# Optimization experiments

Measured on AMD Instinct MI355X. Metric: run time of the kernel, lower is better.

The kernel has to match this reference:

```python
import jax, jax.numpy as jnp
import numpy as np

N_HEAD = 4
GROUPS = 32
EPS = 1e-5


def group_norm(x, scale, bias):
    B, C, H, W = x.shape
    xg = x.reshape(B, GROUPS, C // GROUPS, H, W)
    mu = xg.mean(axis=(2, 3, 4), keepdims=True)
    var = xg.var(axis=(2, 3, 4), keepdims=True)
    xg = (xg - mu) * jax.lax.rsqrt(var + EPS)
    x = xg.reshape(B, C, H, W)
    return x * scale[None, :, None, None] + bias[None, :, None, None]


def setup_inputs() -> dict:
    key = jax.random.key(0)
    k0, k1, k2 = jax.random.split(key, 3)
    B, C, H, W = 2, 64, 64, 64
    x = jax.random.normal(k0, (B, C, H, W), dtype=jnp.float32)
    gn_scale = jnp.ones((C,), dtype=jnp.float32)
    gn_bias = jnp.zeros((C,), dtype=jnp.float32)
    w_qkv = jax.random.normal(k1, (3 * C, C), dtype=jnp.float32) * 0.05  # 1x1 conv, no bias
    w_out = jax.random.normal(k2, (C, C), dtype=jnp.float32) * 0.05     # 1x1 conv
    b_out = jnp.zeros((C,), dtype=jnp.float32)
    return {"x": x, "gn_scale": gn_scale, "gn_bias": gn_bias,
            "w_qkv": w_qkv, "w_out": w_out, "b_out": b_out}


def reference(x, gn_scale, gn_bias, w_qkv, w_out, b_out):
    B, C, H, W = x.shape
    head_dim = C // N_HEAD
    norm = group_norm(x, gn_scale, gn_bias)
    # 1x1 conv == channel matmul
    qkv = jnp.einsum('oc,bchw->bohw', w_qkv, norm)
    qkv = qkv.reshape(B, N_HEAD, head_dim * 3, H, W)
    q, k, v = jnp.split(qkv, 3, axis=2)  # each [B, n, head_dim, H, W]
    # full spatial attention scores, scaled by sqrt(channel) as in source
    attn = jnp.einsum('bnchw,bncyx->bnhwyx', q, k) / jnp.sqrt(jnp.float32(C))
    attn = jax.nn.softmax(attn.reshape(B, N_HEAD, H, W, H * W), axis=-1)
    attn = attn.reshape(B, N_HEAD, H, W, H, W)
    out = jnp.einsum('bnhwyx,bncyx->bnchw', attn, v).reshape(B, C, H, W)
    out = jnp.einsum('oc,bchw->bohw', w_out, out) + b_out[None, :, None, None]
    return out + x
```

## Files before the change

### kernel.cpp

```cpp
#include <hip/hip_runtime.h>
#include <hip/hip_bf16.h>

typedef __attribute__((ext_vector_type(8))) short short8;
typedef __attribute__((ext_vector_type(4))) float f32x4;
typedef __attribute__((ext_vector_type(16))) float f32x16;
typedef __attribute__((ext_vector_type(4))) unsigned int uint4v;

#define DEV static __device__ __forceinline__

DEV unsigned short f2bf(float f){
  unsigned u = __float_as_uint(f);
  u += 0x7fffu + ((u >> 16) & 1u);
  return (unsigned short)(u >> 16);
}

DEV unsigned pack2bf(float a, float b){
  __hip_bfloat162 h = __float22bfloat162_rn(make_float2(a, b));
  unsigned u;
  __builtin_memcpy(&u, &h, 4);
  return u;
}

#define QSCALE 0.180336880111f
#define NSPLIT 8
#define NT 8

__global__ __launch_bounds__(256) void gn_partial_k(const float* __restrict__ x,
                                                    float* __restrict__ gp){
  int blk = blockIdx.x;
  float4 v = ((const float4*)(x + (size_t)blk*1024))[threadIdx.x];
  float s = v.x+v.y+v.z+v.w;
  float q = v.x*v.x+v.y*v.y+v.z*v.z+v.w*v.w;
  #pragma unroll
  for (int off = 1; off < 64; off <<= 1){
    s += __shfl_xor(s, off);
    q += __shfl_xor(q, off);
  }
  __shared__ float red[8];
  int w = threadIdx.x >> 6;
  if ((threadIdx.x & 63) == 0){ red[w*2] = s; red[w*2+1] = q; }
  __syncthreads();
  if (threadIdx.x == 0){
    gp[blk*2+0] = red[0]+red[2]+red[4]+red[6];
    gp[blk*2+1] = red[1]+red[3]+red[5]+red[7];
  }
}

__global__ __launch_bounds__(256) void qkv_k(const float* __restrict__ x,
    const float* __restrict__ gp, const float* __restrict__ gsc,
    const float* __restrict__ gbi, const float* __restrict__ wq,
    unsigned short* __restrict__ q, unsigned short* __restrict__ k,
    unsigned short* __restrict__ vt){
  int b  = blockIdx.x >> 8;
  int s0 = (blockIdx.x & 255) * 16;
  __shared__ float W[192][68];
  __shared__ float A[16][68];
  __shared__ float MS[32][2];
  int t = threadIdx.x;
  for (int i = t; i < 3072; i += 256){
    int o = i >> 4, c4 = (i & 15) * 4;
    *(float4*)&W[o][c4] = ((const float4*)wq)[i];
  }
  if (t < 32){
    float s = 0.f, ss = 0.f;
    #pragma unroll
    for (int i = 0; i < 8; ++i){
      const float* pp = gp + ((b*32 + t)*8 + i)*2;
      s += pp[0]; ss += pp[1];
    }
    float mean = s * (1.f/8192.f);
    MS[t][0] = mean;
    MS[t][1] = rsqrtf(ss * (1.f/8192.f) - mean*mean + 1e-5f);
  }
  __syncthreads();
  {
    int c  = t >> 2;
    int s4 = (t & 3) * 4;
    const float* px = x + ((size_t)b*64 + c)*4096 + s0 + s4;
    float4 v0 = *(const float4*)px;
    float sc = gsc[c] * MS[c>>1][1];
    float bi = gbi[c] - MS[c>>1][0] * sc;
    A[s4+0][c]=v0.x*sc+bi; A[s4+1][c]=v0.y*sc+bi;
    A[s4+2][c]=v0.z*sc+bi; A[s4+3][c]=v0.w*sc+bi;
  }
  __syncthreads();
  int sl = t >> 4, grp = t & 15;
  float acc[12];
  #pragma unroll
  for (int j = 0; j < 12; ++j) acc[j] = 0.f;
  for (int c4 = 0; c4 < 16; ++c4){
    float4 a = *(const float4*)&A[sl][c4*4];
    #pragma unroll
    for (int j = 0; j < 12; ++j){
      float4 wv = *(const float4*)&W[grp + j*16][c4*4];
      acc[j] = fmaf(a.x, wv.x, fmaf(a.y, wv.y, fmaf(a.z, wv.z, fmaf(a.w, wv.w, acc[j]))));
    }
  }
  int s = s0 + sl;
  int slp = (sl & 0x3) | (((sl >> 2) & 1) << 3) | (((sl >> 3) & 1) << 2);
  #pragma unroll
  for (int j = 0; j < 12; ++j){
    int o = grp + j*16;
    int n = o / 48, r = o % 48;
    float val = acc[j];
    if (r < 16){
      q[(((size_t)b*4 + n)*4096 + s)*16 + r] = f2bf(val * QSCALE);
    } else if (r < 32){
      k[(((size_t)b*4 + n)*4096 + s)*16 + r - 16] = f2bf(val);
    } else {
      vt[((size_t)(b*4 + n)*16 + (r - 32))*4096 + s0 + slp] = f2bf(val);
    }
  }
}

__global__ __launch_bounds__(256, 4) void attn_k(const unsigned short* __restrict__ qb,
    const unsigned short* __restrict__ kb, const unsigned short* __restrict__ vt,
    float* __restrict__ part, float* __restrict__ lsums){
  int blk = blockIdx.x;
  int bn = blk & 7;
  int sp = (blk >> 3) & (NSPLIT - 1);
  int qt = blk >> 6;
  int t = threadIdx.x, w = t >> 6, l = t & 63;
  int lq = l & 31, hi = l >> 5;

  const unsigned short* kaddr = kb + ((size_t)bn*4096 + sp*(NT*64) + lq)*16 + hi*8;
  const unsigned short* vaddr = vt + ((size_t)bn*16 + (lq & 15))*4096 + sp*(NT*64) + hi*8;
  bool vld = (lq < 16);
  int qrow = qt*256 + w*64;
  const unsigned short* Qp = qb + ((size_t)bn*4096 + qrow)*16;

  short8 qf0 = *(const short8*)(Qp + (size_t)lq*16 + hi*8);
  short8 qf1 = *(const short8*)(Qp + (size_t)(32 + lq)*16 + hi*8);

  f32x16 O0, O1, zero;
  #pragma unroll
  for (int r = 0; r < 16; ++r){ O0[r] = 0.f; O1[r] = 0.f; zero[r] = 0.f; }

  short8 vsel;
  {
    unsigned short c = (lq == 16) ? (unsigned short)0x3F80 : (unsigned short)0;
    #pragma unroll
    for (int r = 0; r < 8; ++r) vsel[r] = (short)c;
  }

  short8 kf0 = *(const short8*)(kaddr);
  short8 kf1 = *(const short8*)(kaddr + 512);

  #pragma unroll 1
  for (int kt = 0; kt < NT; ++kt){
    short8 v0 = vsel, v1 = vsel, v2 = vsel, v3 = vsel;
    if (vld){
      const unsigned short* va = vaddr + (size_t)kt*64;
      v0 = *(const short8*)(va);
      v1 = *(const short8*)(va + 16);
      v2 = *(const short8*)(va + 32);
      v3 = *(const short8*)(va + 48);
    }
    short8 kn0 = {}, kn1 = {};
    if (kt + 1 < NT){
      const unsigned short* ka = kaddr + (size_t)(kt+1)*1024;
      kn0 = *(const short8*)(ka);
      kn1 = *(const short8*)(ka + 512);
    }

    auto pvstep = [&](f32x16& O, const f32x16& pc, int h8, short8 vf){
      uint4v pw;
      pw[0] = pack2bf(pc[h8+0], pc[h8+1]);
      pw[1] = pack2bf(pc[h8+2], pc[h8+3]);
      pw[2] = pack2bf(pc[h8+4], pc[h8+5]);
      pw[3] = pack2bf(pc[h8+6], pc[h8+7]);
      short8 pa = __builtin_bit_cast(short8, pw);
      O = __builtin_amdgcn_mfma_f32_32x32x16_bf16(pa, vf, O, 0, 0, 0);
    };

    {
      f32x16 sA = __builtin_amdgcn_mfma_f32_32x32x16_bf16(kf0, qf0, zero, 0, 0, 0);
      f32x16 sB = __builtin_amdgcn_mfma_f32_32x32x16_bf16(kf1, qf0, zero, 0, 0, 0);
      #pragma unroll
      for (int r = 0; r < 16; ++r) sA[r] = __builtin_amdgcn_exp2f(sA[r]);
      #pragma unroll
      for (int r = 0; r < 16; ++r) sB[r] = __builtin_amdgcn_exp2f(sB[r]);
      pvstep(O0, sA, 0, v0); pvstep(O0, sA, 8, v1);
      pvstep(O0, sB, 0, v2); pvstep(O0, sB, 8, v3);
    }
    {
      f32x16 sA = __builtin_amdgcn_mfma_f32_32x32x16_bf16(kf0, qf1, zero, 0, 0, 0);
      f32x16 sB = __builtin_amdgcn_mfma_f32_32x32x16_bf16(kf1, qf1, zero, 0, 0, 0);
      #pragma unroll
      for (int r = 0; r < 16; ++r) sA[r] = __builtin_amdgcn_exp2f(sA[r]);
      #pragma unroll
      for (int r = 0; r < 16; ++r) sB[r] = __builtin_amdgcn_exp2f(sB[r]);
      pvstep(O1, sA, 0, v0); pvstep(O1, sA, 8, v1);
      pvstep(O1, sB, 0, v2); pvstep(O1, sB, 8, v3);
    }

    kf0 = kn0; kf1 = kn1;
  }

  float* Op = part + (((size_t)sp*8 + bn)*4096 + qrow)*16;
  size_t lbase = ((size_t)sp*8 + bn)*4096 + qrow;
  #pragma unroll
  for (int r = 0; r < 16; ++r){
    int qr = (r&3) + 8*(r>>2) + 4*hi;
    if (lq < 16){
      __builtin_nontemporal_store(O0[r], &Op[(size_t)qr*16 + lq]);
      __builtin_nontemporal_store(O1[r], &Op[(size_t)(32 + qr)*16 + lq]);
    }
  }
  if (lq == 16){
    #pragma unroll
    for (int r = 0; r < 16; ++r){
      int qr = (r&3) + 8*(r>>2) + 4*hi;
      __builtin_nontemporal_store(O0[r], &lsums[lbase + qr]);
      __builtin_nontemporal_store(O1[r], &lsums[lbase + 32 + qr]);
    }
  }
}

__global__ __launch_bounds__(256) void oproj_k(const float* __restrict__ part,
    const float* __restrict__ lsums, const float* __restrict__ wo,
    const float* __restrict__ bo, const float* __restrict__ x,
    float* __restrict__ out){
  int b  = blockIdx.x >> 8;
  int s0 = (blockIdx.x & 255) * 16;
  __shared__ float W[64][68];
  __shared__ float A[16][68];
  int t = threadIdx.x;
  for (int i = t; i < 1024; i += 256){
    int o = i >> 4, c4 = (i & 15) * 4;
    *(float4*)&W[o][c4] = ((const float4*)wo)[i];
  }
  {
    int sl = t & 15;
    int u  = t >> 4;
    int n = u >> 2, d4 = (u & 3) * 4;
    size_t row = ((size_t)b*4 + n)*4096 + s0 + sl;
    float L = 0.f;
    #pragma unroll
    for (int sp = 0; sp < NSPLIT; ++sp)
      L += __builtin_nontemporal_load(&lsums[(size_t)sp*32768 + row]);
    f32x4 acc = {0.f,0.f,0.f,0.f};
    #pragma unroll
    for (int sp = 0; sp < NSPLIT; ++sp){
      f32x4 u0 = __builtin_nontemporal_load(
          (const f32x4*)(part + ((size_t)sp*32768 + row)*16 + d4));
      acc += u0;
    }
    float inv = 1.f / L;
    A[sl][n*16+d4+0] = acc[0]*inv; A[sl][n*16+d4+1] = acc[1]*inv;
    A[sl][n*16+d4+2] = acc[2]*inv; A[sl][n*16+d4+3] = acc[3]*inv;
  }
  __syncthreads();
  int sl = t & 15, grp = t >> 4;
  float acc[4] = {0.f,0.f,0.f,0.f};
  for (int c4 = 0; c4 < 16; ++c4){
    float4 a = *(const float4*)&A[sl][c4*4];
    #pragma unroll
    for (int j = 0; j < 4; ++j){
      float4 wv = *(const float4*)&W[grp + j*16][c4*4];
      acc[j] = fmaf(a.x, wv.x, fmaf(a.y, wv.y, fmaf(a.z, wv.z, fmaf(a.w, wv.w, acc[j]))));
    }
  }
  int s = s0 + sl;
  #pragma unroll
  for (int j = 0; j < 4; ++j){
    int o = grp + j*16;
    size_t idx = ((size_t)b*64 + o)*4096 + s;
    out[idx] = acc[j] + bo[o] + x[idx];
  }
}

extern "C" void kernel_launch(void* const* d_in, const int* in_sizes, int n_in,
                              void* d_out, int out_size, void* d_ws, size_t ws_size,
                              hipStream_t stream){
  const float* x   = (const float*)d_in[0];
  const float* gsc = (const float*)d_in[1];
  const float* gbi = (const float*)d_in[2];
  const float* wq  = (const float*)d_in[3];
  const float* wo  = (const float*)d_in[4];
  const float* bo  = (const float*)d_in[5];
  float* out = (float*)d_out;

  char* ws = (char*)d_ws;
  float* gp          = (float*)ws;
  unsigned short* q  = (unsigned short*)(ws + 8192);
  unsigned short* k  = (unsigned short*)(ws + 8192 + 1048576);
  unsigned short* vt = (unsigned short*)(ws + 8192 + 2097152);
  float* part        = (float*)(ws + 8192 + 3145728);
  float* lsums       = (float*)(ws + 8192 + 3145728 + 16777216);

  gn_partial_k<<<512,  256, 0, stream>>>(x, gp);
  qkv_k       <<<512,  256, 0, stream>>>(x, gp, gsc, gbi, wq, q, k, vt);
  attn_k      <<<1024, 256, 0, stream>>>(q, k, vt, part, lsums);
  oproj_k     <<<512,  256, 0, stream>>>(part, lsums, wo, bo, x, out);
}
```

Baseline: 58.18 us.

## Stage K/V tiles in LDS and halve the attention key split count

The attention kernel now copies each block's 1024-key K slice and transposed V slice into shared memory, with an XOR swizzle on V. All 8 waves then read K/V from LDS instead of each wave streaming them from global memory. The key split drops from 8 to 4, which halves the partial-output and row-sum buffers that the output projection must reduce. Blocks grow to 512 threads and each wave handles 32 query rows instead of 64. That means one accumulator chain per wave, so there is less MFMA independence to hide latency, and the 64KB of LDS per block limits residency.

```diff
diff --git a/kernel.cpp b/kernel.cpp
--- a/kernel.cpp
+++ b/kernel.cpp
@@ -22,8 +22,8 @@
 }
 
 #define QSCALE 0.180336880111f
-#define NSPLIT 8
-#define NT 8
+#define NSPLIT 4
+#define NT 16
 
 __global__ __launch_bounds__(256) void gn_partial_k(const float* __restrict__ x,
                                                     float* __restrict__ gp){
@@ -113,28 +113,44 @@
   }
 }
 
-__global__ __launch_bounds__(256, 4) void attn_k(const unsigned short* __restrict__ qb,
+__global__ __launch_bounds__(512, 4) void attn_k(const unsigned short* __restrict__ qb,
     const unsigned short* __restrict__ kb, const unsigned short* __restrict__ vt,
     float* __restrict__ part, float* __restrict__ lsums){
   int blk = blockIdx.x;
   int bn = blk & 7;
   int sp = (blk >> 3) & (NSPLIT - 1);
-  int qt = blk >> 6;
+  int qg = blk >> 5;
   int t = threadIdx.x, w = t >> 6, l = t & 63;
   int lq = l & 31, hi = l >> 5;
 
-  const unsigned short* kaddr = kb + ((size_t)bn*4096 + sp*(NT*64) + lq)*16 + hi*8;
-  const unsigned short* vaddr = vt + ((size_t)bn*16 + (lq & 15))*4096 + sp*(NT*64) + hi*8;
-  bool vld = (lq < 16);
-  int qrow = qt*256 + w*64;
-  const unsigned short* Qp = qb + ((size_t)bn*4096 + qrow)*16;
-
-  short8 qf0 = *(const short8*)(Qp + (size_t)lq*16 + hi*8);
-  short8 qf1 = *(const short8*)(Qp + (size_t)(32 + lq)*16 + hi*8);
-
-  f32x16 O0, O1, zero;
-  #pragma unroll
-  for (int r = 0; r < 16; ++r){ O0[r] = 0.f; O1[r] = 0.f; zero[r] = 0.f; }
+  __shared__ unsigned short Klds[16384];
+  __shared__ unsigned short Vlds[16384];
+
+  {
+    const unsigned short* ksrc = kb + ((size_t)bn*4096 + sp*1024)*16;
+    #pragma unroll
+    for (int p = 0; p < 4; ++p){
+      int G = p*512 + t;
+      *(short8*)&Klds[G*8] = *(const short8*)(ksrc + G*8);
+    }
+    const unsigned short* vsrc = vt + (size_t)bn*16*4096 + sp*1024;
+    #pragma unroll
+    for (int p = 0; p < 4; ++p){
+      int G = p*512 + t;
+      int d = G >> 7, gi = G & 127;
+      short8 vv = *(const short8*)(vsrc + (size_t)d*4096 + gi*8);
+      *(short8*)&Vlds[d*1024 + ((gi ^ (d & 7)) * 8)] = vv;
+    }
+  }
+
+  int qrow = qg*256 + w*32;
+  short8 qf = *(const short8*)(qb + ((size_t)bn*4096 + qrow)*16 + (size_t)lq*16 + hi*8);
+
+  __syncthreads();
+
+  f32x16 O, zero;
+  #pragma unroll
+  for (int r = 0; r < 16; ++r){ O[r] = 0.f; zero[r] = 0.f; }
 
   short8 vsel;
   {
@@ -143,27 +159,38 @@
     for (int r = 0; r < 8; ++r) vsel[r] = (short)c;
   }
 
-  short8 kf0 = *(const short8*)(kaddr);
-  short8 kf1 = *(const short8*)(kaddr + 512);
+  int vdrow = (lq & 15);
+  int vxor  = 8 * (vdrow & 7);
+  bool vld = (lq < 16);
+
+  short8 kf0 = *(const short8*)&Klds[(0*64 + 0*32 + lq)*16 + hi*8];
+  short8 kf1 = *(const short8*)&Klds[(0*64 + 1*32 + lq)*16 + hi*8];
 
   #pragma unroll 1
   for (int kt = 0; kt < NT; ++kt){
     short8 v0 = vsel, v1 = vsel, v2 = vsel, v3 = vsel;
     if (vld){
-      const unsigned short* va = vaddr + (size_t)kt*64;
-      v0 = *(const short8*)(va);
-      v1 = *(const short8*)(va + 16);
-      v2 = *(const short8*)(va + 32);
-      v3 = *(const short8*)(va + 48);
+      int base = vdrow*1024 + kt*64 + hi*8;
+      v0 = *(const short8*)&Vlds[(base +  0) ^ vxor];
+      v1 = *(const short8*)&Vlds[(base + 16) ^ vxor];
+      v2 = *(const short8*)&Vlds[(base + 32) ^ vxor];
+      v3 = *(const short8*)&Vlds[(base + 48) ^ vxor];
     }
     short8 kn0 = {}, kn1 = {};
     if (kt + 1 < NT){
-      const unsigned short* ka = kaddr + (size_t)(kt+1)*1024;
-      kn0 = *(const short8*)(ka);
-      kn1 = *(const short8*)(ka + 512);
-    }
-
-    auto pvstep = [&](f32x16& O, const f32x16& pc, int h8, short8 vf){
+      kn0 = *(const short8*)&Klds[((kt+1)*64 + lq)*16 + hi*8];
+      kn1 = *(const short8*)&Klds[((kt+1)*64 + 32 + lq)*16 + hi*8];
+    }
+
+    f32x16 sA = __builtin_amdgcn_mfma_f32_32x32x16_bf16(kf0, qf, zero, 0, 0, 0);
+    f32x16 sB = __builtin_amdgcn_mfma_f32_32x32x16_bf16(kf1, qf, zero, 0, 0, 0);
+
+    #pragma unroll
+    for (int r = 0; r < 16; ++r) sA[r] = __builtin_amdgcn_exp2f(sA[r]);
+    #pragma unroll
+    for (int r = 0; r < 16; ++r) sB[r] = __builtin_amdgcn_exp2f(sB[r]);
+
+    auto pvstep = [&](const f32x16& pc, int h8, short8 vf){
       uint4v pw;
       pw[0] = pack2bf(pc[h8+0], pc[h8+1]);
       pw[1] = pack2bf(pc[h8+2], pc[h8+3]);
@@ -172,27 +199,10 @@
       short8 pa = __builtin_bit_cast(short8, pw);
       O = __builtin_amdgcn_mfma_f32_32x32x16_bf16(pa, vf, O, 0, 0, 0);
     };
-
-    {
-      f32x16 sA = __builtin_amdgcn_mfma_f32_32x32x16_bf16(kf0, qf0, zero, 0, 0, 0);
-      f32x16 sB = __builtin_amdgcn_mfma_f32_32x32x16_bf16(kf1, qf0, zero, 0, 0, 0);
-      #pragma unroll
-      for (int r = 0; r < 16; ++r) sA[r] = __builtin_amdgcn_exp2f(sA[r]);
-      #pragma unroll
-      for (int r = 0; r < 16; ++r) sB[r] = __builtin_amdgcn_exp2f(sB[r]);
-      pvstep(O0, sA, 0, v0); pvstep(O0, sA, 8, v1);
-      pvstep(O0, sB, 0, v2); pvstep(O0, sB, 8, v3);
-    }
-    {
-      f32x16 sA = __builtin_amdgcn_mfma_f32_32x32x16_bf16(kf0, qf1, zero, 0, 0, 0);
-      f32x16 sB = __builtin_amdgcn_mfma_f32_32x32x16_bf16(kf1, qf1, zero, 0, 0, 0);
-      #pragma unroll
-      for (int r = 0; r < 16; ++r) sA[r] = __builtin_amdgcn_exp2f(sA[r]);
-      #pragma unroll
-      for (int r = 0; r < 16; ++r) sB[r] = __builtin_amdgcn_exp2f(sB[r]);
-      pvstep(O1, sA, 0, v0); pvstep(O1, sA, 8, v1);
-      pvstep(O1, sB, 0, v2); pvstep(O1, sB, 8, v3);
-    }
+    pvstep(sA, 0, v0);
+    pvstep(sA, 8, v1);
+    pvstep(sB, 0, v2);
+    pvstep(sB, 8, v3);
 
     kf0 = kn0; kf1 = kn1;
   }
@@ -202,17 +212,13 @@
   #pragma unroll
   for (int r = 0; r < 16; ++r){
     int qr = (r&3) + 8*(r>>2) + 4*hi;
-    if (lq < 16){
-      __builtin_nontemporal_store(O0[r], &Op[(size_t)qr*16 + lq]);
-      __builtin_nontemporal_store(O1[r], &Op[(size_t)(32 + qr)*16 + lq]);
-    }
+    if (lq < 16) __builtin_nontemporal_store(O[r], &Op[(size_t)qr*16 + lq]);
   }
   if (lq == 16){
     #pragma unroll
     for (int r = 0; r < 16; ++r){
       int qr = (r&3) + 8*(r>>2) + 4*hi;
-      __builtin_nontemporal_store(O0[r], &lsums[lbase + qr]);
-      __builtin_nontemporal_store(O1[r], &lsums[lbase + 32 + qr]);
+      __builtin_nontemporal_store(O[r], &lsums[lbase + qr]);
     }
   }
 }
@@ -287,10 +293,10 @@
   unsigned short* k  = (unsigned short*)(ws + 8192 + 1048576);
   unsigned short* vt = (unsigned short*)(ws + 8192 + 2097152);
   float* part        = (float*)(ws + 8192 + 3145728);
-  float* lsums       = (float*)(ws + 8192 + 3145728 + 16777216);
-
-  gn_partial_k<<<512,  256, 0, stream>>>(x, gp);
-  qkv_k       <<<512,  256, 0, stream>>>(x, gp, gsc, gbi, wq, q, k, vt);
-  attn_k      <<<1024, 256, 0, stream>>>(q, k, vt, part, lsums);
-  oproj_k     <<<512,  256, 0, stream>>>(part, lsums, wo, bo, x, out);
-}
+  float* lsums       = (float*)(ws + 8192 + 3145728 + 8388608);
+
+  gn_partial_k<<<512, 256, 0, stream>>>(x, gp);
+  qkv_k       <<<512, 256, 0, stream>>>(x, gp, gsc, gbi, wq, q, k, vt);
+  attn_k      <<<512, 512, 0, stream>>>(q, k, vt, part, lsums);
+  oproj_k     <<<512, 256, 0, stream>>>(part, lsums, wo, bo, x, out);
+}
```

Measured after the change: 57.07 us. Within noise of the previous version (-1.9%).
